# Kernel tuning notes

Measured on AMD Instinct MI355X. Metric: run time of the kernel, lower is better.

Reference implementation:

```python
import jax, jax.numpy as jnp
import numpy as np

B, C_IN, C_MID, C_OUT, H, W = 256, 2, 128, 64, 15, 15
N_RES = 4  # line_length//2 - 1 with line_length=11

# per-direction input offsets for kernel taps w0 and w2 (w1 is always center),
# matching fix_direction_order=True sparse 3x3 kernel construction:
# dir0 horizontal, dir1 vertical, dir2 anti-diagonal, dir3 main diagonal.
OFFSETS = (((0, -1), (0, 1)),
           ((-1, 0), (1, 0)),
           ((1, -1), (-1, 1)),
           ((-1, -1), (1, 1)))


def shift2d(x, di, dj):
    # out[..., i, j] = x[..., i+di, j+dj] with zero padding (di,dj in {-1,0,1})
    nd = x.ndim
    xp = jnp.pad(x, [(0, 0)] * (nd - 2) + [(1, 1), (1, 1)])
    h, w = x.shape[-2], x.shape[-1]
    return xp[..., 1 + di:1 + di + h, 1 + dj:1 + dj + w]


def dir_conv(x, w, b):
    # x: [4,B,Cin,H,W]; w: [Cout,Cin,3]; b: [Cout]
    x0 = jnp.stack([shift2d(x[d], *OFFSETS[d][0]) for d in range(4)])
    x2 = jnp.stack([shift2d(x[d], *OFFSETS[d][1]) for d in range(4)])
    y = (jnp.einsum('oc,dbchw->dbohw', w[..., 0], x0)
         + jnp.einsum('oc,dbchw->dbohw', w[..., 1], x)
         + jnp.einsum('oc,dbchw->dbohw', w[..., 2], x2))
    return y + b[None, None, :, None, None]


def conv1x1(x, w, b):
    # x: [4,B,Cin,H,W]; w: [Cout,Cin]; b: [Cout]
    return jnp.einsum('oc,dbchw->dbohw', w, x) + b[None, None, :, None, None]


def setup_inputs() -> dict:
    key = jax.random.key(0)
    ks = jax.random.split(key, 16)
    s_in = 1.0 / np.sqrt(3 * C_IN)
    s_mid = 1.0 / np.sqrt(3 * C_MID)
    s_pw = 1.0 / np.sqrt(C_MID)
    return {
        'x': jax.random.normal(ks[0], (B, C_IN, H, W), jnp.float32),
        'dconv0_w': jax.random.normal(ks[1], (C_MID, C_IN, 3), jnp.float32) * s_in,
        'dconv0_b': jnp.zeros((C_MID,), jnp.float32),
        'res_dconv_w': jax.random.normal(ks[2], (N_RES, C_MID, C_MID, 3), jnp.float32) * s_mid,
        'res_dconv_b': jnp.zeros((N_RES, C_MID), jnp.float32),
        'res_pw_w': jax.random.normal(ks[3], (N_RES, C_MID, C_MID), jnp.float32) * s_pw,
        'res_pw_b': jnp.zeros((N_RES, C_MID), jnp.float32),
        'c0_w1': jax.random.normal(ks[4], (C_MID, C_MID), jnp.float32) * s_pw,
        'c0_b1': jnp.zeros((C_MID,), jnp.float32),
        'c0_w2': jax.random.normal(ks[5], (C_MID, C_MID), jnp.float32) * s_pw,
        'c0_b2': jnp.zeros((C_MID,), jnp.float32),
        'final_w': jax.random.normal(ks[6], (C_OUT, C_MID), jnp.float32) * s_pw,
        'final_b': jnp.zeros((C_OUT,), jnp.float32),
    }


def reference(x, dconv0_w, dconv0_b, res_dconv_w, res_dconv_b,
              res_pw_w, res_pw_b, c0_w1, c0_b1, c0_w2, c0_b2,
              final_w, final_b):
    act = jax.nn.silu
    # all 4 direction streams start from the same input plane
    h = jnp.broadcast_to(x[None], (4,) + x.shape)  # [4,B,Cin,H,W]
    h = act(dir_conv(h, dconv0_w, dconv0_b))
    # DirectionalConvResBlocks (norm='none')
    for i in range(N_RES):
        r = h
        h = act(dir_conv(h, res_dconv_w[i], res_dconv_b[i]))
        h = act(conv1x1(h, res_pw_w[i], res_pw_b[i]))
        h = h + r
    # Conv0dResBlock (two 1x1 convs, middle_dim_multipler=1)
    r = h
    h = act(conv1x1(h, c0_w1, c0_b1))
    h = act(conv1x1(h, c0_w2, c0_b2))
    h = h + r
    # final 1x1 conv, then stack directions at dim=1 -> [B,4,Cout,H,W]
    h = conv1x1(h, final_w, final_b)
    return jnp.transpose(h, (1, 0, 2, 3, 4))
```

## Files before the change

kernel.cpp:

```cpp
#include <hip/hip_runtime.h>

using u16 = unsigned short;
using u32 = unsigned int;

typedef __bf16 bf16x8 __attribute__((ext_vector_type(8)));
typedef float  f32x4  __attribute__((ext_vector_type(4)));

#define NPOS   225
#define NT     15
#define ROWP   136
#define A_ROWS 289
#define B_ROWS 241
#define A_ELEMS (A_ROWS*ROWP)
#define B_ELEMS (B_ROWS*ROWP)
#define LDS_BYTES ((A_ELEMS + B_ELEMS)*2)
#define RSTRIDE17 (17*ROWP)

#define WA_PER_L 49152
#define WP_OFF   (4*WA_PER_L)
#define WP_PER   16384
#define WF_OFF   (WP_OFF + 6*WP_PER)
#define W_U16_TOTAL (WF_OFF + 8192)

__device__ __forceinline__ float bflo(u32 q){ return __uint_as_float(q << 16); }
__device__ __forceinline__ float bfhi(u32 q){ return __uint_as_float(q & 0xffff0000u); }
__device__ __forceinline__ u16 f2bf(float f){
  u32 u = __float_as_uint(f);
  return (u16)((u + 0x7fffu + ((u >> 16) & 1u)) >> 16);
}
__device__ __forceinline__ u32 packbf(float a, float b){
  union { __bf16 h[2]; u32 u; } r;
  r.h[0] = (__bf16)a; r.h[1] = (__bf16)b;
  return r.u;
}
__device__ __forceinline__ float silu_f(float x){
  return x * __builtin_amdgcn_rcpf(1.f + __expf(-x));
}
__device__ __forceinline__ f32x4 mfma16(bf16x8 a, bf16x8 b, f32x4 c){
  return __builtin_amdgcn_mfma_f32_16x16x32_bf16(a, b, c, 0, 0, 0);
}

__global__ void prep_w(const float* __restrict__ d0w, const float* __restrict__ rdw,
                       const float* __restrict__ rpw, const float* __restrict__ c1w,
                       const float* __restrict__ c2w, const float* __restrict__ fw,
                       float* __restrict__ ws)
{
  u16* wsb = (u16*)(ws + 768);
  const int total = 768 + W_U16_TOTAL;
  for (int idx = blockIdx.x*blockDim.x + threadIdx.x; idx < total; idx += gridDim.x*blockDim.x){
    if (idx < 768){
      int k = idx >> 7, o = idx & 127;
      ws[idx] = d0w[o*6 + k];
      continue;
    }
    int e = idx - 768;
    float v;
    if (e < WP_OFF){
      int L = e / WA_PER_L, r = e % WA_PER_L;
      int w = r / 6144, r2 = r % 6144;
      int t = r2 >> 11, r3 = r2 & 2047;
      int kb = r3 >> 9, r4 = r3 & 511;
      int l = r4 >> 3, j = r4 & 7;
      int o = w*16 + (l & 15);
      int c = kb*32 + ((l >> 4) << 3) + j;
      v = rdw[((L*128 + o)*128 + c)*3 + t];
    } else if (e < WF_OFF){
      int t2 = e - WP_OFF;
      int i = t2 / WP_PER, r = t2 % WP_PER;
      int w = r >> 11, r2 = r & 2047;
      int kb = r2 >> 9, r3 = r2 & 511;
      int l = r3 >> 3, j = r3 & 7;
      int o = w*16 + (l & 15);
      int c = kb*32 + ((l >> 4) << 3) + j;
      v = (i < 4) ? rpw[(i*128 + o)*128 + c]
        : (i == 4) ? c1w[o*128 + c] : c2w[o*128 + c];
    } else {
      int e2 = e - WF_OFF;
      int ot = e2 >> 11, r = e2 & 2047;
      int kb = r >> 9, r2 = r & 511;
      int l = r2 >> 3, j = r2 & 7;
      int o = ot*16 + (l & 15);
      int c = kb*32 + ((l >> 4) << 3) + j;
      v = fw[o*128 + c];
    }
    wsb[e] = f2bf(v);
  }
}

__device__ __forceinline__ void dconv_mfma(const u16* __restrict__ As, u16* __restrict__ Bs,
    const u16* __restrict__ wloc, const float* __restrict__ bias,
    int lane, int og, int T0, int T1, int off0, int off2)
{
  const int col = lane & 15, kg = lane >> 4, koff = kg*8;
  bf16x8 wa[2][12];
  #pragma unroll
  for (int ot=0; ot<2; ++ot)
    #pragma unroll
    for (int f=0; f<12; ++f)
      wa[ot][f] = *(const bf16x8*)(wloc + (2*og+ot)*6144 + f*512 + lane*8);
  f32x4 bz0 = *(const f32x4*)(bias + og*32 + kg*4);
  f32x4 bz1 = *(const f32x4*)(bias + og*32 + 16 + kg*4);
  const int c1 = (col+1)*ROWP;
  #pragma unroll 1
  for (int tile=T0; tile<T1; ++tile){
    int rb = (tile+1)*RSTRIDE17 + c1;
    const u16* s0 = As + rb + off0 + koff;
    const u16* s1 = As + rb + koff;
    const u16* s2 = As + rb + off2 + koff;
    f32x4 a0 = bz0, a1 = bz1;
    __builtin_amdgcn_s_setprio(1);
    #pragma unroll
    for (int kb=0; kb<4; ++kb){
      bf16x8 v0 = *(const bf16x8*)(s0 + kb*32);
      bf16x8 v1 = *(const bf16x8*)(s1 + kb*32);
      bf16x8 v2 = *(const bf16x8*)(s2 + kb*32);
      a0 = mfma16(wa[0][kb],   v0, a0); a1 = mfma16(wa[1][kb],   v0, a1);
      a0 = mfma16(wa[0][4+kb], v1, a0); a1 = mfma16(wa[1][4+kb], v1, a1);
      a0 = mfma16(wa[0][8+kb], v2, a0); a1 = mfma16(wa[1][8+kb], v2, a1);
    }
    __builtin_amdgcn_s_setprio(0);
    if (col < 15){
      u16* dp = Bs + (tile*16+col)*ROWP + og*32 + kg*4;
      uint2 w0; w0.x = packbf(silu_f(a0[0]), silu_f(a0[1]));
      w0.y = packbf(silu_f(a0[2]), silu_f(a0[3]));
      *(uint2*)dp = w0;
      uint2 w1; w1.x = packbf(silu_f(a1[0]), silu_f(a1[1]));
      w1.y = packbf(silu_f(a1[2]), silu_f(a1[3]));
      *(uint2*)(dp+16) = w1;
    }
  }
}

template<bool SRC_HALO, bool DST_HALO, bool RESID>
__device__ __forceinline__ void pw_mfma(const u16* __restrict__ src, u16* __restrict__ dst,
    const u16* __restrict__ wloc, const float* __restrict__ bias,
    int lane, int og2, int T0, int T1)
{
  const int col = lane & 15, kg = lane >> 4, koff = kg*8;
  bf16x8 wp[4][4];
  #pragma unroll
  for (int ot=0; ot<4; ++ot)
    #pragma unroll
    for (int kb=0; kb<4; ++kb)
      wp[ot][kb] = *(const bf16x8*)(wloc + (og2*4+ot)*2048 + kb*512 + lane*8);
  f32x4 bz[4];
  #pragma unroll
  for (int ot=0; ot<4; ++ot) bz[ot] = *(const f32x4*)(bias + og2*64 + ot*16 + kg*4);
  const int chb = og2*64 + kg*4;
  const int c1 = (col+1)*ROWP;
  #pragma unroll 2
  for (int tile=T0; tile<T1; ++tile){
    const int rh = (tile+1)*RSTRIDE17 + c1;
    const int rc = (tile*16+col)*ROWP;
    const u16* S = src + (SRC_HALO ? rh : rc) + koff;
    f32x4 a0 = bz[0], a1 = bz[1], a2 = bz[2], a3 = bz[3];
    __builtin_amdgcn_s_setprio(1);
    #pragma unroll
    for (int kb=0; kb<4; ++kb){
      bf16x8 v = *(const bf16x8*)(S + kb*32);
      a0 = mfma16(wp[0][kb], v, a0);
      a1 = mfma16(wp[1][kb], v, a1);
      a2 = mfma16(wp[2][kb], v, a2);
      a3 = mfma16(wp[3][kb], v, a3);
    }
    __builtin_amdgcn_s_setprio(0);
    if (col < 15){
      u16* dp = dst + (DST_HALO ? rh : rc) + chb;
      f32x4 aa[4] = {a0, a1, a2, a3};
      #pragma unroll
      for (int ot=0; ot<4; ++ot){
        u16* dq = dp + ot*16;
        float s0 = silu_f(aa[ot][0]), s1 = silu_f(aa[ot][1]);
        float s2 = silu_f(aa[ot][2]), s3 = silu_f(aa[ot][3]);
        if (RESID){
          uint2 r = *(const uint2*)dq;
          s0 += bflo(r.x); s1 += bfhi(r.x); s2 += bflo(r.y); s3 += bfhi(r.y);
        }
        uint2 w0v; w0v.x = packbf(s0, s1); w0v.y = packbf(s2, s3);
        *(uint2*)dq = w0v;
      }
    }
  }
}

__device__ __forceinline__ void fin_mfma(const u16* __restrict__ As,
    const u16* __restrict__ wloc, const float* __restrict__ bias,
    float* __restrict__ out, int lane, int ogf, int T0, int T1, int bd)
{
  const int col = lane & 15, kg = lane >> 4, koff = kg*8;
  bf16x8 wf[2][4];
  #pragma unroll
  for (int ot=0; ot<2; ++ot)
    #pragma unroll
    for (int kb=0; kb<4; ++kb)
      wf[ot][kb] = *(const bf16x8*)(wloc + (ogf*2+ot)*2048 + kb*512 + lane*8);
  f32x4 bz0 = *(const f32x4*)(bias + ogf*32 + kg*4);
  f32x4 bz1 = *(const f32x4*)(bias + ogf*32 + 16 + kg*4);
  const int c1 = (col+1)*ROWP;
  #pragma unroll 1
  for (int tile=T0; tile<T1; ++tile){
    const u16* S = As + (tile+1)*RSTRIDE17 + c1 + koff;
    f32x4 a0 = bz0, a1 = bz1;
    __builtin_amdgcn_s_setprio(1);
    #pragma unroll
    for (int kb=0; kb<4; ++kb){
      bf16x8 v = *(const bf16x8*)(S + kb*32);
      a0 = mfma16(wf[0][kb], v, a0);
      a1 = mfma16(wf[1][kb], v, a1);
    }
    __builtin_amdgcn_s_setprio(0);
    if (col < 15){
      float* op = out + ((size_t)(bd*64 + ogf*32 + kg*4))*NPOS + tile*15 + col;
      op[0]      = a0[0];
      op[NPOS]   = a0[1];
      op[2*NPOS] = a0[2];
      op[3*NPOS] = a0[3];
      float* oq = op + 16*NPOS;
      oq[0]      = a1[0];
      oq[NPOS]   = a1[1];
      oq[2*NPOS] = a1[2];
      oq[3*NPOS] = a1[3];
    }
  }
}

__global__ void __launch_bounds__(512, 2)
mix9_main(const float* __restrict__ x,
          const float* __restrict__ b_d0,
          const float* __restrict__ b_rd,
          const float* __restrict__ b_rp,
          const float* __restrict__ b_c1,
          const float* __restrict__ b_c2,
          const float* __restrict__ b_fin,
          const float* __restrict__ wt,
          float* __restrict__ out)
{
  extern __shared__ u16 sm[];
  u16* As = sm;
  u16* Bs = sm + A_ELEMS;

  const int blk  = blockIdx.x;
  const int b    = blk >> 2, d = blk & 3;
  const int tid  = threadIdx.x;
  const int wave = __builtin_amdgcn_readfirstlane(tid >> 6);
  const int lane = tid & 63;

  const int ogd  = wave >> 1;
  const int phd  = wave & 1;
  const int T0d  = phd * 8;
  const int T1d  = phd ? NT : 8;
  const int og2  = wave >> 2;
  const int ph4  = wave & 3;
  const int T0p  = ph4 * 4;
  const int T1p  = (ph4 == 3) ? NT : T0p + 4;
  const int ob   = wave * 16;

  const int DI0[4] = {0,-1, 1,-1}, DJ0[4] = {-1, 0,-1,-1};
  const int DI2[4] = {0, 1,-1, 1}, DJ2[4] = { 1, 0, 1, 1};
  const int di0 = DI0[d], dj0 = DJ0[d], di2 = DI2[d], dj2 = DJ2[d];
  const int off0 = (di0*17 + dj0)*ROWP;
  const int off2 = (di2*17 + dj2)*ROWP;

  for (int k2 = tid; k2 < A_ELEMS; k2 += 512) As[k2] = 0;
  float* xs = (float*)Bs;
  for (int k2 = tid; k2 < 2*NPOS; k2 += 512) xs[k2] = x[b*(2*NPOS) + k2];
  __syncthreads();

  #pragma unroll 1
  for (int pb = 0; pb < 4; ++pb){
    int pp = pb*64 + lane;
    int i = pp >> 4, j = pp & 15;
    if (i >= 15 || j >= 15) continue;
    float acc[16];
    #pragma unroll
    for (int oo=0;oo<16;++oo) acc[oo] = b_d0[ob+oo];
    #pragma unroll
    for (int c=0;c<2;++c){
      int i0=i+di0, j0=j+dj0, i2=i+di2, j2=j+dj2;
      float x0 = ((unsigned)i0<15u && (unsigned)j0<15u) ? xs[c*NPOS + i0*15 + j0] : 0.f;
      float x1 = xs[c*NPOS + i*15 + j];
      float x2 = ((unsigned)i2<15u && (unsigned)j2<15u) ? xs[c*NPOS + i2*15 + j2] : 0.f;
      const float* w0r = wt + (c*3+0)*128 + ob;
      const float* w1r = wt + (c*3+1)*128 + ob;
      const float* w2r = wt + (c*3+2)*128 + ob;
      #pragma unroll
      for (int oo=0;oo<16;++oo)
        acc[oo] = fmaf(w0r[oo],x0, fmaf(w1r[oo],x1, fmaf(w2r[oo],x2, acc[oo])));
    }
    u16* dp = As + ((i+1)*17 + (j+1))*ROWP + ob;
    #pragma unroll
    for (int oo=0;oo<16;oo+=2)
      *(u32*)(dp+oo) = packbf(silu_f(acc[oo]), silu_f(acc[oo+1]));
  }
  __syncthreads();

  const u16* wsb = (const u16*)(wt + 768);

  #pragma unroll 1
  for (int L = 0; L < 4; ++L){
    dconv_mfma(As, Bs, wsb + L*WA_PER_L, b_rd + L*128, lane, ogd, T0d, T1d, off0, off2);
    __syncthreads();
    pw_mfma<false,true,true>(Bs, As, wsb + WP_OFF + L*WP_PER, b_rp + L*128, lane, og2, T0p, T1p);
    __syncthreads();
  }

  pw_mfma<true,false,false>(As, Bs, wsb + WP_OFF + 4*WP_PER, b_c1, lane, og2, T0p, T1p);
  __syncthreads();
  pw_mfma<false,true,true>(Bs, As, wsb + WP_OFF + 5*WP_PER, b_c2, lane, og2, T0p, T1p);
  __syncthreads();

  fin_mfma(As, wsb + WF_OFF, b_fin, out, lane, og2, T0p, T1p, b*4 + d);
}

extern "C" void kernel_launch(void* const* d_in, const int* in_sizes, int n_in,
                              void* d_out, int out_size, void* d_ws, size_t ws_size,
                              hipStream_t stream)
{
  const float* x     = (const float*)d_in[0];
  const float* w_d0  = (const float*)d_in[1];
  const float* b_d0  = (const float*)d_in[2];
  const float* w_rd  = (const float*)d_in[3];
  const float* b_rd  = (const float*)d_in[4];
  const float* w_rp  = (const float*)d_in[5];
  const float* b_rp  = (const float*)d_in[6];
  const float* w_c1  = (const float*)d_in[7];
  const float* b_c1  = (const float*)d_in[8];
  const float* w_c2  = (const float*)d_in[9];
  const float* b_c2  = (const float*)d_in[10];
  const float* w_fin = (const float*)d_in[11];
  const float* b_fin = (const float*)d_in[12];
  float* wt  = (float*)d_ws;
  float* out = (float*)d_out;

  prep_w<<<128, 512, 0, stream>>>(w_d0, w_rd, w_rp, w_c1, w_c2, w_fin, wt);

  (void)hipFuncSetAttribute((const void*)mix9_main,
                            hipFuncAttributeMaxDynamicSharedMemorySize, LDS_BYTES);
  mix9_main<<<1024, 512, LDS_BYTES, stream>>>(x, b_d0, b_rd, b_rp, b_c1, b_c2, b_fin, wt, out);
}
```

Baseline: 244.0 us.

## Restructure directional conv to 64-channel waves with tap-outer loop and permuted channels

The directional conv now gives each wave 64 output channels over 3-4 position tiles, looping taps outermost so only one tap's weights (16 fragments) are live at a time. This replaces 24 resident weight fragments per wave reused across 8 tiles. It also permutes channel order in prep so each lane's MFMA output maps to 16 contiguous bf16 channels, turning the LDS stores and residual reads into 128-bit accesses instead of 64-bit ones. In exchange each wave holds more accumulator registers and reloads weights per tap, and the conv0 bias is moved into the workspace in permuted order.

```diff
diff --git a/kernel.cpp b/kernel.cpp
--- a/kernel.cpp
+++ b/kernel.cpp
@@ -22,6 +22,10 @@
 #define WF_OFF   (WP_OFF + 6*WP_PER)
 #define W_U16_TOTAL (WF_OFF + 8192)
 
+__host__ __device__ __forceinline__ int permc(int c){
+  return (c & ~0x3C) | (((c >> 2) & 3) << 4) | (((c >> 4) & 3) << 2);
+}
+
 __device__ __forceinline__ float bflo(u32 q){ return __uint_as_float(q << 16); }
 __device__ __forceinline__ float bfhi(u32 q){ return __uint_as_float(q & 0xffff0000u); }
 __device__ __forceinline__ u16 f2bf(float f){
@@ -40,93 +44,110 @@
   return __builtin_amdgcn_mfma_f32_16x16x32_bf16(a, b, c, 0, 0, 0);
 }
 
-__global__ void prep_w(const float* __restrict__ d0w, const float* __restrict__ rdw,
+__global__ void prep_w(const float* __restrict__ d0w, const float* __restrict__ d0b,
+                       const float* __restrict__ rdw,
                        const float* __restrict__ rpw, const float* __restrict__ c1w,
                        const float* __restrict__ c2w, const float* __restrict__ fw,
                        float* __restrict__ ws)
 {
-  u16* wsb = (u16*)(ws + 768);
-  const int total = 768 + W_U16_TOTAL;
+  u16* wsb = (u16*)(ws + 896);
+  const int total = 896 + W_U16_TOTAL;
   for (int idx = blockIdx.x*blockDim.x + threadIdx.x; idx < total; idx += gridDim.x*blockDim.x){
     if (idx < 768){
-      int k = idx >> 7, o = idx & 127;
-      ws[idx] = d0w[o*6 + k];
+      int k = idx >> 7, s = idx & 127;
+      ws[idx] = d0w[permc(s)*6 + k];
       continue;
     }
-    int e = idx - 768;
+    if (idx < 896){
+      int s = idx - 768;
+      ws[idx] = d0b[permc(s)];
+      continue;
+    }
+    int e = idx - 896;
     float v;
     if (e < WP_OFF){
       int L = e / WA_PER_L, r = e % WA_PER_L;
-      int w = r / 6144, r2 = r % 6144;
-      int t = r2 >> 11, r3 = r2 & 2047;
-      int kb = r3 >> 9, r4 = r3 & 511;
-      int l = r4 >> 3, j = r4 & 7;
-      int o = w*16 + (l & 15);
-      int c = kb*32 + ((l >> 4) << 3) + j;
-      v = rdw[((L*128 + o)*128 + c)*3 + t];
+      int og = r / 24576; int r1 = r - og*24576;
+      int tap = r1 >> 13; int r2 = r1 & 8191;
+      int ot = r2 >> 11, kb = (r2 >> 9) & 3, l = (r2 >> 3) & 63, j = r2 & 7;
+      int o = (og*4 + ot)*16 + (l & 15);
+      int ks = kb*32 + ((l >> 4) << 3) + j;
+      v = rdw[((L*128 + o)*128 + permc(ks))*3 + tap];
     } else if (e < WF_OFF){
       int t2 = e - WP_OFF;
       int i = t2 / WP_PER, r = t2 % WP_PER;
-      int w = r >> 11, r2 = r & 2047;
-      int kb = r2 >> 9, r3 = r2 & 511;
-      int l = r3 >> 3, j = r3 & 7;
-      int o = w*16 + (l & 15);
-      int c = kb*32 + ((l >> 4) << 3) + j;
-      v = (i < 4) ? rpw[(i*128 + o)*128 + c]
-        : (i == 4) ? c1w[o*128 + c] : c2w[o*128 + c];
+      int og2 = r >> 13;
+      int ot = (r >> 11) & 3, kb = (r >> 9) & 3, l = (r >> 3) & 63, j = r & 7;
+      int o = (og2*4 + ot)*16 + (l & 15);
+      int ks = kb*32 + ((l >> 4) << 3) + j;
+      v = (i < 4) ? rpw[(i*128 + o)*128 + permc(ks)]
+        : (i == 4) ? c1w[o*128 + permc(ks)] : c2w[o*128 + permc(ks)];
     } else {
       int e2 = e - WF_OFF;
-      int ot = e2 >> 11, r = e2 & 2047;
-      int kb = r >> 9, r2 = r & 511;
-      int l = r2 >> 3, j = r2 & 7;
+      int ot = e2 >> 11, kb = (e2 >> 9) & 3, l = (e2 >> 3) & 63, j = e2 & 7;
       int o = ot*16 + (l & 15);
-      int c = kb*32 + ((l >> 4) << 3) + j;
-      v = fw[o*128 + c];
+      int ks = kb*32 + ((l >> 4) << 3) + j;
+      v = fw[o*128 + permc(ks)];
     }
     wsb[e] = f2bf(v);
   }
 }
 
+__device__ __forceinline__ uint4 pack_silu2(const f32x4& a, const f32x4& b){
+  uint4 q;
+  q.x = packbf(silu_f(a[0]), silu_f(a[1]));
+  q.y = packbf(silu_f(a[2]), silu_f(a[3]));
+  q.z = packbf(silu_f(b[0]), silu_f(b[1]));
+  q.w = packbf(silu_f(b[2]), silu_f(b[3]));
+  return q;
+}
+
+template<int NTL>
 __device__ __forceinline__ void dconv_mfma(const u16* __restrict__ As, u16* __restrict__ Bs,
     const u16* __restrict__ wloc, const float* __restrict__ bias,
-    int lane, int og, int T0, int T1, int off0, int off2)
+    int lane, int og, int T0, int off0, int off2)
 {
   const int col = lane & 15, kg = lane >> 4, koff = kg*8;
-  bf16x8 wa[2][12];
+  f32x4 acc[4][NTL];
   #pragma unroll
-  for (int ot=0; ot<2; ++ot)
-    #pragma unroll
-    for (int f=0; f<12; ++f)
-      wa[ot][f] = *(const bf16x8*)(wloc + (2*og+ot)*6144 + f*512 + lane*8);
-  f32x4 bz0 = *(const f32x4*)(bias + og*32 + kg*4);
-  f32x4 bz1 = *(const f32x4*)(bias + og*32 + 16 + kg*4);
-  const int c1 = (col+1)*ROWP;
+  for (int ot=0; ot<4; ++ot){
+    f32x4 bz = *(const f32x4*)(bias + og*64 + ot*16 + kg*4);
+    #pragma unroll
+    for (int t=0;t<NTL;++t) acc[ot][t] = bz;
+  }
+  const int c1 = (col+1)*ROWP + koff;
   #pragma unroll 1
-  for (int tile=T0; tile<T1; ++tile){
-    int rb = (tile+1)*RSTRIDE17 + c1;
-    const u16* s0 = As + rb + off0 + koff;
-    const u16* s1 = As + rb + koff;
-    const u16* s2 = As + rb + off2 + koff;
-    f32x4 a0 = bz0, a1 = bz1;
-    __builtin_amdgcn_s_setprio(1);
-    #pragma unroll
-    for (int kb=0; kb<4; ++kb){
-      bf16x8 v0 = *(const bf16x8*)(s0 + kb*32);
-      bf16x8 v1 = *(const bf16x8*)(s1 + kb*32);
-      bf16x8 v2 = *(const bf16x8*)(s2 + kb*32);
-      a0 = mfma16(wa[0][kb],   v0, a0); a1 = mfma16(wa[1][kb],   v0, a1);
-      a0 = mfma16(wa[0][4+kb], v1, a0); a1 = mfma16(wa[1][4+kb], v1, a1);
-      a0 = mfma16(wa[0][8+kb], v2, a0); a1 = mfma16(wa[1][8+kb], v2, a1);
-    }
-    __builtin_amdgcn_s_setprio(0);
-    if (col < 15){
-      u16* dp = Bs + (tile*16+col)*ROWP + og*32 + kg*4;
-      uint2 w0; w0.x = packbf(silu_f(a0[0]), silu_f(a0[1]));
-      w0.y = packbf(silu_f(a0[2]), silu_f(a0[3]));
-      *(uint2*)dp = w0;
-      uint2 w1; w1.x = packbf(silu_f(a1[0]), silu_f(a1[1]));
-      w1.y = packbf(silu_f(a1[2]), silu_f(a1[3]));
-      *(uint2*)(dp+16) = w1;
+  for (int tap=0; tap<3; ++tap){
+    const int offr = (tap==0) ? off0 : (tap==1) ? 0 : off2;
+    bf16x8 w[4][4];
+    #pragma unroll
+    for (int ot=0; ot<4; ++ot)
+      #pragma unroll
+      for (int kb=0; kb<4; ++kb)
+        w[ot][kb] = *(const bf16x8*)(wloc + tap*8192 + ot*2048 + kb*512 + lane*8);
+    #pragma unroll
+    for (int t=0; t<NTL; ++t){
+      const u16* s = As + (T0+t+1)*RSTRIDE17 + c1 + offr;
+      __builtin_amdgcn_s_setprio(1);
+      #pragma unroll
+      for (int kb=0; kb<4; ++kb){
+        bf16x8 v = *(const bf16x8*)(s + kb*32);
+        acc[0][t] = mfma16(w[0][kb], v, acc[0][t]);
+        acc[1][t] = mfma16(w[1][kb], v, acc[1][t]);
+        acc[2][t] = mfma16(w[2][kb], v, acc[2][t]);
+        acc[3][t] = mfma16(w[3][kb], v, acc[3][t]);
+      }
+      __builtin_amdgcn_s_setprio(0);
+    }
+  }
+  if (col < 15){
+    #pragma unroll
+    for (int t=0;t<NTL;++t){
+      u16* dp = Bs + ((T0+t)*16+col)*ROWP + og*64 + kg*16;
+      uint4 q0 = pack_silu2(acc[0][t], acc[1][t]);
+      uint4 q1 = pack_silu2(acc[2][t], acc[3][t]);
+      *(uint4*)dp = q0;
+      *(uint4*)(dp+8) = q1;
     }
   }
 }
@@ -142,11 +163,10 @@
   for (int ot=0; ot<4; ++ot)
     #pragma unroll
     for (int kb=0; kb<4; ++kb)
-      wp[ot][kb] = *(const bf16x8*)(wloc + (og2*4+ot)*2048 + kb*512 + lane*8);
+      wp[ot][kb] = *(const bf16x8*)(wloc + og2*8192 + ot*2048 + kb*512 + lane*8);
   f32x4 bz[4];
   #pragma unroll
   for (int ot=0; ot<4; ++ot) bz[ot] = *(const f32x4*)(bias + og2*64 + ot*16 + kg*4);
-  const int chb = og2*64 + kg*4;
   const int c1 = (col+1)*ROWP;
   #pragma unroll 2
   for (int tile=T0; tile<T1; ++tile){
@@ -165,20 +185,26 @@
     }
     __builtin_amdgcn_s_setprio(0);
     if (col < 15){
-      u16* dp = dst + (DST_HALO ? rh : rc) + chb;
-      f32x4 aa[4] = {a0, a1, a2, a3};
-      #pragma unroll
-      for (int ot=0; ot<4; ++ot){
-        u16* dq = dp + ot*16;
-        float s0 = silu_f(aa[ot][0]), s1 = silu_f(aa[ot][1]);
-        float s2 = silu_f(aa[ot][2]), s3 = silu_f(aa[ot][3]);
-        if (RESID){
-          uint2 r = *(const uint2*)dq;
-          s0 += bflo(r.x); s1 += bfhi(r.x); s2 += bflo(r.y); s3 += bfhi(r.y);
-        }
-        uint2 w0v; w0v.x = packbf(s0, s1); w0v.y = packbf(s2, s3);
-        *(uint2*)dq = w0v;
+      u16* dp = dst + (DST_HALO ? rh : rc) + og2*64 + kg*16;
+      float s0 = silu_f(a0[0]), s1 = silu_f(a0[1]), s2 = silu_f(a0[2]), s3 = silu_f(a0[3]);
+      float s4 = silu_f(a1[0]), s5 = silu_f(a1[1]), s6 = silu_f(a1[2]), s7 = silu_f(a1[3]);
+      float s8 = silu_f(a2[0]), s9 = silu_f(a2[1]), sa = silu_f(a2[2]), sb = silu_f(a2[3]);
+      float sc = silu_f(a3[0]), sd = silu_f(a3[1]), se = silu_f(a3[2]), sf = silu_f(a3[3]);
+      if (RESID){
+        uint4 r0 = *(const uint4*)dp;
+        uint4 r1 = *(const uint4*)(dp+8);
+        s0 += bflo(r0.x); s1 += bfhi(r0.x); s2 += bflo(r0.y); s3 += bfhi(r0.y);
+        s4 += bflo(r0.z); s5 += bfhi(r0.z); s6 += bflo(r0.w); s7 += bfhi(r0.w);
+        s8 += bflo(r1.x); s9 += bfhi(r1.x); sa += bflo(r1.y); sb += bfhi(r1.y);
+        sc += bflo(r1.z); sd += bfhi(r1.z); se += bflo(r1.w); sf += bfhi(r1.w);
       }
+      uint4 q0, q1;
+      q0.x = packbf(s0, s1); q0.y = packbf(s2, s3);
+      q0.z = packbf(s4, s5); q0.w = packbf(s6, s7);
+      q1.x = packbf(s8, s9); q1.y = packbf(sa, sb);
+      q1.z = packbf(sc, sd); q1.w = packbf(se, sf);
+      *(uint4*)dp = q0;
+      *(uint4*)(dp+8) = q1;
     }
   }
 }
@@ -226,7 +252,6 @@
 
 __global__ void __launch_bounds__(512, 2)
 mix9_main(const float* __restrict__ x,
-          const float* __restrict__ b_d0,
           const float* __restrict__ b_rd,
           const float* __restrict__ b_rp,
           const float* __restrict__ b_c1,
@@ -245,10 +270,8 @@
   const int wave = __builtin_amdgcn_readfirstlane(tid >> 6);
   const int lane = tid & 63;
 
-  const int ogd  = wave >> 1;
-  const int phd  = wave & 1;
-  const int T0d  = phd * 8;
-  const int T1d  = phd ? NT : 8;
+  const int ogd  = wave >> 2;
+  const int pgd  = wave & 3;
   const int og2  = wave >> 2;
   const int ph4  = wave & 3;
   const int T0p  = ph4 * 4;
@@ -266,6 +289,7 @@
   for (int k2 = tid; k2 < 2*NPOS; k2 += 512) xs[k2] = x[b*(2*NPOS) + k2];
   __syncthreads();
 
+  const float* b0p = wt + 768;
   #pragma unroll 1
   for (int pb = 0; pb < 4; ++pb){
     int pp = pb*64 + lane;
@@ -273,7 +297,7 @@
     if (i >= 15 || j >= 15) continue;
     float acc[16];
     #pragma unroll
-    for (int oo=0;oo<16;++oo) acc[oo] = b_d0[ob+oo];
+    for (int oo=0;oo<16;++oo) acc[oo] = b0p[ob+oo];
     #pragma unroll
     for (int c=0;c<2;++c){
       int i0=i+di0, j0=j+dj0, i2=i+di2, j2=j+dj2;
@@ -294,11 +318,14 @@
   }
   __syncthreads();
 
-  const u16* wsb = (const u16*)(wt + 768);
+  const u16* wsb = (const u16*)(wt + 896);
 
   #pragma unroll 1
   for (int L = 0; L < 4; ++L){
-    dconv_mfma(As, Bs, wsb + L*WA_PER_L, b_rd + L*128, lane, ogd, T0d, T1d, off0, off2);
+    if (pgd == 3)
+      dconv_mfma<3>(As, Bs, wsb + L*WA_PER_L + ogd*24576, b_rd + L*128, lane, ogd, 12, off0, off2);
+    else
+      dconv_mfma<4>(As, Bs, wsb + L*WA_PER_L + ogd*24576, b_rd + L*128, lane, ogd, pgd*4, off0, off2);
     __syncthreads();
     pw_mfma<false,true,true>(Bs, As, wsb + WP_OFF + L*WP_PER, b_rp + L*128, lane, og2, T0p, T1p);
     __syncthreads();
@@ -332,9 +359,9 @@
   float* wt  = (float*)d_ws;
   float* out = (float*)d_out;
 
-  prep_w<<<128, 512, 0, stream>>>(w_d0, w_rd, w_rp, w_c1, w_c2, w_fin, wt);
+  prep_w<<<128, 512, 0, stream>>>(w_d0, b_d0, w_rd, w_rp, w_c1, w_c2, w_fin, wt);
 
   (void)hipFuncSetAttribute((const void*)mix9_main,
                             hipFuncAttributeMaxDynamicSharedMemorySize, LDS_BYTES);
-  mix9_main<<<1024, 512, LDS_BYTES, stream>>>(x, b_d0, b_rd, b_rp, b_c1, b_c2, b_fin, wt, out);
-}
+  mix9_main<<<1024, 512, LDS_BYTES, stream>>>(x, b_rd, b_rp, b_c1, b_c2, b_fin, wt, out);
+}
```

New measurement: 243.5 us. Within noise of the previous version (-0.2%).
